# Performance work log

Measured on AMD Instinct MI355X. Metric: run time of the kernel, lower is better.

Reference implementation:

```python
import jax, jax.numpy as jnp
import numpy as np

IN_C = 16
OUT_C = 16
GRID = 8
K = 3  # spline order
RANGE = (-1.0, 1.0)
COEF_M = GRID + K                       # number of B-spline coefficients per (in,out)
SIZE = IN_C * OUT_C * COEF_M + 2 * IN_C * OUT_C  # 3328: coef + univariate_w + residual_w


def _grid():
    # extended knot grid: grid_size intervals over RANGE, padded by K on each side
    h = (RANGE[1] - RANGE[0]) / GRID
    return (np.arange(-K, GRID + K + 1) * h + RANGE[0]).astype(np.float32)


def b_splines(x, grid):
    # x: (N, in) -> bases: (N, in, GRID + K) via Cox-de Boor recursion
    xg = x[..., None]
    bases = ((xg >= grid[:-1]) & (xg < grid[1:])).astype(x.dtype)
    for p in range(1, K + 1):
        left = (xg - grid[:-(p + 1)]) / (grid[p:-1] - grid[:-(p + 1)])
        right = (grid[p + 1:] - xg) / (grid[p + 1:] - grid[1:-p])
        bases = left * bases[..., :-1] + right * bases[..., 1:]
    return bases


def setup_inputs() -> dict:
    key = jax.random.key(0)
    k1, k2 = jax.random.split(key)
    x = jax.random.normal(k1, (2, IN_C, 128, 128), jnp.float32)
    w = jax.random.normal(k2, (2, SIZE, 128, 128), jnp.float32) * 0.1
    return {"x": x, "w": w}


def reference(x, w):
    B, C, H, W = x.shape
    N = B * H * W
    # per-pixel dynamic KAN parameters
    wt = jnp.transpose(w, (0, 2, 3, 1)).reshape(N, SIZE)
    xt = jnp.transpose(x, (0, 2, 3, 1)).reshape(N, IN_C)
    i0 = IN_C * OUT_C * COEF_M
    i1 = i0 + IN_C * OUT_C
    coef = wt[:, :i0].reshape(N, IN_C, OUT_C, COEF_M)
    uw = wt[:, i0:i1].reshape(N, IN_C, OUT_C)
    rw = wt[:, i1:].reshape(N, IN_C, OUT_C)
    grid = jnp.asarray(_grid())
    bases = b_splines(xt, grid)                    # (N, in, M)
    spline = jnp.einsum('niom,nim->nio', coef, bases)  # per-token spline values
    y = jnp.einsum('nio,nio->no', uw, spline) + jnp.einsum('nio,ni->no', rw, jax.nn.silu(xt))
    return jnp.transpose(y.reshape(B, H, W, OUT_C), (0, 3, 1, 2))
```

## Files before the change

### kernel.cpp

```cpp
#include <hip/hip_runtime.h>

#define IN_C   16
#define OUT_C  16
#define COEF_M 11
#define PLANE  16384
#define WSIZE  3328
#define I0     2816
#define I1     3072

__global__ __launch_bounds__(256) void kan_kernel(
    const float* __restrict__ x, const float* __restrict__ w,
    float* __restrict__ out)
{
    const int tid = threadIdx.x;
    const int px  = tid & 63;
    const int g   = tid >> 6;
    const int pixel = blockIdx.x * 64 + px;
    const int b  = pixel >> 14;
    const int hw = pixel & (PLANE - 1);

    const float* wb = w + (size_t)b * WSIZE * PLANE + hw;
    const float* xb = x + (size_t)b * IN_C * PLANE + hw;

    float acc[OUT_C];
    #pragma unroll
    for (int o = 0; o < OUT_C; ++o) acc[o] = 0.0f;

    for (int ii = 0; ii < 4; ++ii) {
        const int i = g * 4 + ii;
        const float xi = xb[(size_t)i * PLANE];

        float bp[14];
        #pragma unroll
        for (int j = 0; j < 14; ++j) {
            const float tj  = -1.75f + 0.25f * j;
            const float tj1 = tj + 0.25f;
            bp[j] = (xi >= tj && xi < tj1) ? 1.0f : 0.0f;
        }
        #pragma unroll
        for (int p = 1; p <= 3; ++p) {
            const float inv = 1.0f / (0.25f * (float)p);
            #pragma unroll
            for (int j = 0; j < 14 - p; ++j) {
                const float tj    = -1.75f + 0.25f * j;
                const float left  = (xi - tj) * inv;
                const float right = ((tj + 0.25f * (float)(p + 1)) - xi) * inv;
                bp[j] = left * bp[j] + right * bp[j + 1];
            }
        }

        const float sx = xi / (1.0f + __expf(-xi));

        const float* ci = wb + (size_t)(i * (OUT_C * COEF_M)) * PLANE;
        const float* ui = wb + (size_t)(I0 + i * OUT_C) * PLANE;
        const float* ri = wb + (size_t)(I1 + i * OUT_C) * PLANE;

        #pragma unroll
        for (int o = 0; o < OUT_C; ++o) {
            const float* c = ci + (size_t)(o * COEF_M) * PLANE;
            float sp = 0.0f;
            #pragma unroll
            for (int m = 0; m < COEF_M; ++m)
                sp += c[(size_t)m * PLANE] * bp[m];
            acc[o] += ui[(size_t)o * PLANE] * sp + ri[(size_t)o * PLANE] * sx;
        }
    }

    __shared__ float red[4 * 64 * 17];
    #pragma unroll
    for (int o = 0; o < OUT_C; ++o)
        red[(g * 64 + px) * 17 + o] = acc[o];
    __syncthreads();

    const int og = g;
    #pragma unroll
    for (int k = 0; k < 4; ++k) {
        const int o = og * 4 + k;
        const float s = red[(0 * 64 + px) * 17 + o]
                      + red[(1 * 64 + px) * 17 + o]
                      + red[(2 * 64 + px) * 17 + o]
                      + red[(3 * 64 + px) * 17 + o];
        out[(size_t)b * (OUT_C * PLANE) + (size_t)o * PLANE + hw] = s;
    }
}

extern "C" void kernel_launch(void* const* d_in, const int* in_sizes, int n_in,
                              void* d_out, int out_size, void* d_ws, size_t ws_size,
                              hipStream_t stream) {
    const float* x = (const float*)d_in[0];
    const float* w = (const float*)d_in[1];
    float* out = (float*)d_out;

    kan_kernel<<<dim3(512), dim3(256), 0, stream>>>(x, w, out);
}
```

Baseline: 562.5 us.

## Assign one input channel per thread with two pixels via float2 loads

```diff
diff --git a/kernel.cpp b/kernel.cpp
--- a/kernel.cpp
+++ b/kernel.cpp
@@ -8,79 +8,93 @@
 #define I0     2816
 #define I1     3072
 
-__global__ __launch_bounds__(256) void kan_kernel(
+__global__ __launch_bounds__(256, 4) void kan_kernel(
     const float* __restrict__ x, const float* __restrict__ w,
     float* __restrict__ out)
 {
     const int tid = threadIdx.x;
-    const int px  = tid & 63;
-    const int g   = tid >> 6;
-    const int pixel = blockIdx.x * 64 + px;
-    const int b  = pixel >> 14;
-    const int hw = pixel & (PLANE - 1);
+    const int pp  = tid & 15;
+    const int i   = tid >> 4;
+    const int pixel0 = blockIdx.x * 32 + pp * 2;
+    const int b  = pixel0 >> 14;
+    const int hw = pixel0 & (PLANE - 1);
 
     const float* wb = w + (size_t)b * WSIZE * PLANE + hw;
     const float* xb = x + (size_t)b * IN_C * PLANE + hw;
 
-    float acc[OUT_C];
+    const float2 x2 = *(const float2*)(xb + (size_t)i * PLANE);
+
+    float bpa[14], bpb[14];
     #pragma unroll
-    for (int o = 0; o < OUT_C; ++o) acc[o] = 0.0f;
-
-    for (int ii = 0; ii < 4; ++ii) {
-        const int i = g * 4 + ii;
-        const float xi = xb[(size_t)i * PLANE];
-
-        float bp[14];
+    for (int j = 0; j < 14; ++j) {
+        const float tj  = -1.75f + 0.25f * j;
+        const float tj1 = tj + 0.25f;
+        bpa[j] = (x2.x >= tj && x2.x < tj1) ? 1.0f : 0.0f;
+        bpb[j] = (x2.y >= tj && x2.y < tj1) ? 1.0f : 0.0f;
+    }
+    #pragma unroll
+    for (int p = 1; p <= 3; ++p) {
+        const float inv = 1.0f / (0.25f * (float)p);
         #pragma unroll
-        for (int j = 0; j < 14; ++j) {
+        for (int j = 0; j < 14 - p; ++j) {
             const float tj  = -1.75f + 0.25f * j;
-            const float tj1 = tj + 0.25f;
-            bp[j] = (xi >= tj && xi < tj1) ? 1.0f : 0.0f;
-        }
-        #pragma unroll
-        for (int p = 1; p <= 3; ++p) {
-            const float inv = 1.0f / (0.25f * (float)p);
-            #pragma unroll
-            for (int j = 0; j < 14 - p; ++j) {
-                const float tj    = -1.75f + 0.25f * j;
-                const float left  = (xi - tj) * inv;
-                const float right = ((tj + 0.25f * (float)(p + 1)) - xi) * inv;
-                bp[j] = left * bp[j] + right * bp[j + 1];
-            }
-        }
-
-        const float sx = xi / (1.0f + __expf(-xi));
-
-        const float* ci = wb + (size_t)(i * (OUT_C * COEF_M)) * PLANE;
-        const float* ui = wb + (size_t)(I0 + i * OUT_C) * PLANE;
-        const float* ri = wb + (size_t)(I1 + i * OUT_C) * PLANE;
-
-        #pragma unroll
-        for (int o = 0; o < OUT_C; ++o) {
-            const float* c = ci + (size_t)(o * COEF_M) * PLANE;
-            float sp = 0.0f;
-            #pragma unroll
-            for (int m = 0; m < COEF_M; ++m)
-                sp += c[(size_t)m * PLANE] * bp[m];
-            acc[o] += ui[(size_t)o * PLANE] * sp + ri[(size_t)o * PLANE] * sx;
+            const float tp1 = tj + 0.25f * (float)(p + 1);
+            const float la = (x2.x - tj) * inv;
+            const float ra = (tp1 - x2.x) * inv;
+            bpa[j] = la * bpa[j] + ra * bpa[j + 1];
+            const float lb = (x2.y - tj) * inv;
+            const float rb = (tp1 - x2.y) * inv;
+            bpb[j] = lb * bpb[j] + rb * bpb[j + 1];
         }
     }
 
-    __shared__ float red[4 * 64 * 17];
+    const float sxa = x2.x / (1.0f + __expf(-x2.x));
+    const float sxb = x2.y / (1.0f + __expf(-x2.y));
+
+    const float* ci = wb + (size_t)(i * (OUT_C * COEF_M)) * PLANE;
+    const float* ui = wb + (size_t)(I0 + i * OUT_C) * PLANE;
+    const float* ri = wb + (size_t)(I1 + i * OUT_C) * PLANE;
+
+    float acca[OUT_C], accb[OUT_C];
     #pragma unroll
-    for (int o = 0; o < OUT_C; ++o)
-        red[(g * 64 + px) * 17 + o] = acc[o];
+    for (int o = 0; o < OUT_C; ++o) {
+        const float* c = ci + (size_t)(o * COEF_M) * PLANE;
+        float spa = 0.0f, spb = 0.0f;
+        #pragma unroll
+        for (int m = 0; m < COEF_M; ++m) {
+            const float2 cv = *(const float2*)(c + (size_t)m * PLANE);
+            spa += cv.x * bpa[m];
+            spb += cv.y * bpb[m];
+        }
+        const float2 uv = *(const float2*)(ui + (size_t)o * PLANE);
+        const float2 rv = *(const float2*)(ri + (size_t)o * PLANE);
+        acca[o] = uv.x * spa + rv.x * sxa;
+        accb[o] = uv.y * spb + rv.y * sxb;
+    }
+
+    __shared__ float red[16 * 16 * 33];
+    const int row = (i * 16 + pp) * 33;
+    #pragma unroll
+    for (int o = 0; o < OUT_C; ++o) {
+        red[row + 2 * o]     = acca[o];
+        red[row + 2 * o + 1] = accb[o];
+    }
     __syncthreads();
 
-    const int og = g;
+    const int px = tid & 31;
+    const int og = tid >> 5;
+    const int rp = (px >> 1) * 33 + (px & 1);
+    const int pixel = blockIdx.x * 32 + px;
+    const int ob = pixel >> 14;
+    const int ohw = pixel & (PLANE - 1);
     #pragma unroll
-    for (int k = 0; k < 4; ++k) {
-        const int o = og * 4 + k;
-        const float s = red[(0 * 64 + px) * 17 + o]
-                      + red[(1 * 64 + px) * 17 + o]
-                      + red[(2 * 64 + px) * 17 + o]
-                      + red[(3 * 64 + px) * 17 + o];
-        out[(size_t)b * (OUT_C * PLANE) + (size_t)o * PLANE + hw] = s;
+    for (int k = 0; k < 2; ++k) {
+        const int o = og * 2 + k;
+        float s = 0.0f;
+        #pragma unroll
+        for (int g2 = 0; g2 < 16; ++g2)
+            s += red[g2 * (16 * 33) + rp + 2 * o];
+        out[(size_t)ob * (OUT_C * PLANE) + (size_t)o * PLANE + ohw] = s;
     }
 }
 
@@ -91,5 +105,5 @@
     const float* w = (const float*)d_in[1];
     float* out = (float*)d_out;
 
-    kan_kernel<<<dim3(512), dim3(256), 0, stream>>>(x, w, out);
+    kan_kernel<<<dim3(1024), dim3(256), 0, stream>>>(x, w, out);
 }
```

Result: slower. 574.9 us (+2.2%).
